# Kernel optimization log

Measured on AMD Instinct MI355X. Metric: run time of the kernel, lower is better.

## Reference

```python
import jax, jax.numpy as jnp
import numpy as np

B, T, S = 8, 8192, 128
VD, LD, E, H = 256, 768, 256, 8
HD = E // H
SCALE = HD ** -0.5
NEG = -9e15


def setup_inputs() -> dict:
    key = jax.random.key(0)
    ks = jax.random.split(key, 16)
    def xavier(k, shape):
        fan_in, fan_out = shape[1], shape[0]
        lim = np.sqrt(6.0 / (fan_in + fan_out))
        return jax.random.uniform(k, shape, jnp.float32, -lim, lim)
    return {
        "v": jax.random.normal(ks[0], (B, T, VD), jnp.float32),
        "l": jax.random.normal(ks[1], (B, S, LD), jnp.float32),
        "v_pos": jax.random.normal(ks[2], (B, T, VD), jnp.float32),
        "attention_mask_l": jnp.ones((B, S), jnp.int32),
        "attention_mask_v": jnp.ones((B, T), jnp.int32),
        "Wv": xavier(ks[3], (E, VD)),  "bv": jnp.zeros((E,), jnp.float32),
        "Wl": xavier(ks[4], (E, LD)),  "bl": jnp.zeros((E,), jnp.float32),
        "Wvv": xavier(ks[5], (E, VD)), "bvv": jnp.zeros((E,), jnp.float32),
        "Wvl": xavier(ks[6], (E, LD)), "bvl": jnp.zeros((E,), jnp.float32),
        "Wov": xavier(ks[7], (VD, E)), "bov": jnp.zeros((VD,), jnp.float32),
        "Wol": xavier(ks[8], (LD, E)), "bol": jnp.zeros((LD,), jnp.float32),
    }


def _heads(x):  # [B, N, E] -> [B, H, N, HD]
    Bn, N, _ = x.shape
    return x.reshape(Bn, N, H, HD).transpose(0, 2, 1, 3)


def reference(v, l, v_pos, attention_mask_l, attention_mask_v,
              Wv, bv, Wl, bl, Wvv, bvv, Wvl, bvl, Wov, bov, Wol, bol):
    # projections
    q = _heads(((v + v_pos) @ Wv.T + bv) * SCALE)   # [B,H,T,HD]
    k = _heads(l @ Wl.T + bl)                        # [B,H,S,HD]
    val_v = _heads(v @ Wvv.T + bvv)                  # [B,H,T,HD]
    val_l = _heads(l @ Wvl.T + bvl)                  # [B,H,S,HD]

    # shared score matrix
    attn = jnp.einsum("bhtd,bhsd->bhts", q, k)       # [B,H,T,S]

    # language -> vision direction (softmax over vision tokens T)
    attn_T = attn.transpose(0, 1, 3, 2)              # [B,H,S,T]
    attn_l = attn_T - jnp.max(attn_T, axis=-1, keepdims=True)
    mv = attention_mask_v.astype(jnp.float32)
    add_v = jnp.where(mv == 0, NEG, mv)[:, None, None, :]  # [B,1,1,T]
    attn_l = jax.nn.softmax(attn_l + add_v, axis=-1)

    # vision -> language direction (softmax over language tokens S)
    ml = attention_mask_l.astype(jnp.float32)
    add_l = jnp.where(ml == 0, NEG, ml)[:, None, None, :]  # [B,1,1,S]
    attn_v = jax.nn.softmax(attn + add_l, axis=-1)

    # dropout p=0.1 is identity in eval mode
    out_v = jnp.einsum("bhts,bhsd->bhtd", attn_v, val_l)  # [B,H,T,HD]
    out_l = jnp.einsum("bhst,bhtd->bhsd", attn_l, val_v)  # [B,H,S,HD]

    out_v = out_v.transpose(0, 2, 1, 3).reshape(B, T, E) @ Wov.T + bov
    out_l = out_l.transpose(0, 2, 1, 3).reshape(B, S, E) @ Wol.T + bol
    return out_v, out_l
```

## Files before the change

kernel.cpp:

```cpp
#include <hip/hip_runtime.h>

#define B_ 8
#define T_ 8192
#define S_ 128
#define VD_ 256
#define LD_ 768
#define E_ 256
#define H_ 8
#define HD_ 32
#define TC_ 8
#define SCALE_ 0.17677669529663687f
#define NEG_ -9.0e15f

typedef __bf16 bf16x8 __attribute__((ext_vector_type(8)));
typedef float f32x4 __attribute__((ext_vector_type(4)));
typedef unsigned int uint4v __attribute__((ext_vector_type(4)));

__device__ inline float bf2f(unsigned short u) {
    return __uint_as_float(((unsigned int)u) << 16);
}
__device__ inline unsigned short f2bf(float f) {
    unsigned int u = __float_as_uint(f);
    u = u + 0x7FFFu + ((u >> 16) & 1u);
    return (unsigned short)(u >> 16);
}
__device__ inline bf16x8 lds8(const unsigned short* p) {
    uint4v v = *reinterpret_cast<const uint4v*>(p);
    return __builtin_bit_cast(bf16x8, v);
}

template<typename T>
__device__ inline uint4v load8_as_bf16(const T* p);

template<> __device__ inline uint4v load8_as_bf16<unsigned short>(const unsigned short* p) {
    return *reinterpret_cast<const uint4v*>(p);
}
template<> __device__ inline uint4v load8_as_bf16<float>(const float* p) {
    f32x4 f0 = reinterpret_cast<const f32x4*>(p)[0];
    f32x4 f1 = reinterpret_cast<const f32x4*>(p)[1];
    uint4v r;
    #pragma unroll
    for (int jj = 0; jj < 2; ++jj) {
        r[jj]     = (unsigned int)f2bf(f0[jj*2]) | ((unsigned int)f2bf(f0[jj*2+1]) << 16);
        r[jj + 2] = (unsigned int)f2bf(f1[jj*2]) | ((unsigned int)f2bf(f1[jj*2+1]) << 16);
    }
    return r;
}
__device__ inline uint4v load8_add_as_bf16(const float* p, const float* p2) {
    f32x4 a0 = reinterpret_cast<const f32x4*>(p)[0];
    f32x4 a1 = reinterpret_cast<const f32x4*>(p)[1];
    f32x4 b0 = reinterpret_cast<const f32x4*>(p2)[0];
    f32x4 b1 = reinterpret_cast<const f32x4*>(p2)[1];
    a0 += b0; a1 += b1;
    uint4v r;
    #pragma unroll
    for (int jj = 0; jj < 2; ++jj) {
        r[jj]     = (unsigned int)f2bf(a0[jj*2]) | ((unsigned int)f2bf(a0[jj*2+1]) << 16);
        r[jj + 2] = (unsigned int)f2bf(a1[jj*2]) | ((unsigned int)f2bf(a1[jj*2+1]) << 16);
    }
    return r;
}

template<typename TA, typename TW, typename TOUT, bool HAS_A2, bool SCALED>
__global__ __launch_bounds__(256) void gemm_bt(
    const TA* __restrict__ A, const TA* __restrict__ A2,
    const TW* __restrict__ W, const float* __restrict__ bias,
    TOUT* __restrict__ C, int M, int N, int K, float scale)
{
    __shared__ __align__(16) unsigned short As[64][72];
    __shared__ __align__(16) unsigned short Ws[64][72];
    const int tid  = threadIdx.x;
    const int lane = tid & 63;
    const int w    = tid >> 6;
    const int wm   = w >> 1, wn = w & 1;
    const int m0   = blockIdx.x * 64, n0 = blockIdx.y * 64;
    const int row  = tid >> 2, c0 = tid & 3;
    const int qd   = lane >> 4, lr = lane & 15;
    const f32x4 zero = {0.f, 0.f, 0.f, 0.f};
    f32x4 acc[2][2] = {{zero, zero}, {zero, zero}};

    for (int k0 = 0; k0 < K; k0 += 64) {
        #pragma unroll
        for (int cc = 0; cc < 2; ++cc) {
            int c = c0 + cc * 4;
            const TA* pa = A + (size_t)(m0 + row) * K + k0 + c * 8;
            uint4v va;
            if constexpr (HAS_A2) {
                const TA* pa2 = A2 + (size_t)(m0 + row) * K + k0 + c * 8;
                va = load8_add_as_bf16(pa, pa2);
            } else {
                va = load8_as_bf16<TA>(pa);
            }
            *reinterpret_cast<uint4v*>(&As[row][c * 8]) = va;
            const TW* pw = W + (size_t)(n0 + row) * K + k0 + c * 8;
            *reinterpret_cast<uint4v*>(&Ws[row][c * 8]) = load8_as_bf16<TW>(pw);
        }
        __syncthreads();
        #pragma unroll
        for (int ks = 0; ks < 2; ++ks) {
            bf16x8 af[2], bfr[2];
            #pragma unroll
            for (int i = 0; i < 2; ++i)
                af[i] = lds8(&As[wm * 32 + i * 16 + lr][ks * 32 + qd * 8]);
            #pragma unroll
            for (int i = 0; i < 2; ++i)
                bfr[i] = lds8(&Ws[wn * 32 + i * 16 + lr][ks * 32 + qd * 8]);
            #pragma unroll
            for (int i = 0; i < 2; ++i)
                #pragma unroll
                for (int j = 0; j < 2; ++j)
                    acc[i][j] = __builtin_amdgcn_mfma_f32_16x16x32_bf16(
                        af[i], bfr[j], acc[i][j], 0, 0, 0);
        }
        __syncthreads();
    }
    #pragma unroll
    for (int j = 0; j < 2; ++j) {
        int col = n0 + wn * 32 + j * 16 + lr;
        float bval = bias[col];
        #pragma unroll
        for (int i = 0; i < 2; ++i) {
            int r0 = m0 + wm * 32 + i * 16 + qd * 4;
            #pragma unroll
            for (int r = 0; r < 4; ++r) {
                float v = acc[i][j][r] + bval;
                if (SCALED) v *= scale;
                if constexpr (sizeof(TOUT) == 2)
                    C[(size_t)(r0 + r) * N + col] = (TOUT)f2bf(v);
                else
                    C[(size_t)(r0 + r) * N + col] = (TOUT)v;
            }
        }
    }
}

__global__ __launch_bounds__(256) void attn_v_kernel(
    const unsigned short* __restrict__ q, const unsigned short* __restrict__ k,
    const unsigned short* __restrict__ vall, const int* __restrict__ mask_l,
    unsigned short* __restrict__ hv)
{
    __shared__ __align__(16) unsigned short Pl[64][136];
    __shared__ __align__(16) unsigned short Vt[32][136];
    const int tid  = threadIdx.x;
    const int lane = tid & 63;
    const int w    = tid >> 6;
    const int bh   = blockIdx.y, b = bh >> 3, h = bh & 7;
    const int t0   = blockIdx.x * 64;
    const int quad = lane >> 4, lr = lane & 15;
    const f32x4 zero = {0.f, 0.f, 0.f, 0.f};

    {
        int s = tid >> 1, dh = (tid & 1) * 16;
        const unsigned short* p = vall + (size_t)(b * S_ + s) * E_ + h * HD_ + dh;
        #pragma unroll
        for (int part = 0; part < 2; ++part) {
            uint4v v = reinterpret_cast<const uint4v*>(p)[part];
            #pragma unroll
            for (int jj = 0; jj < 4; ++jj) {
                unsigned int u = v[jj];
                int d = dh + part * 8 + jj * 2;
                Vt[d][s]     = (unsigned short)(u & 0xffffu);
                Vt[d + 1][s] = (unsigned short)(u >> 16);
            }
        }
    }

    bf16x8 afq = lds8(q + (size_t)(b * T_ + t0 + w * 16 + lr) * E_ + h * HD_ + quad * 8);
    f32x4 sc[8];
    #pragma unroll
    for (int n = 0; n < 8; ++n) {
        bf16x8 bk = lds8(k + (size_t)(b * S_ + n * 16 + lr) * E_ + h * HD_ + quad * 8);
        sc[n] = __builtin_amdgcn_mfma_f32_16x16x32_bf16(afq, bk, zero, 0, 0, 0);
    }
    #pragma unroll
    for (int n = 0; n < 8; ++n) {
        int s = n * 16 + lr;
        int mv = mask_l[b * S_ + s];
        float ad = (mv == 0) ? NEG_ : (float)mv;
        #pragma unroll
        for (int r = 0; r < 4; ++r) sc[n][r] += ad;
    }
    #pragma unroll
    for (int r = 0; r < 4; ++r) {
        float m = -3.0e38f;
        #pragma unroll
        for (int n = 0; n < 8; ++n) m = fmaxf(m, sc[n][r]);
        for (int off = 1; off < 16; off <<= 1) m = fmaxf(m, __shfl_xor(m, off));
        float sum = 0.f;
        #pragma unroll
        for (int n = 0; n < 8; ++n) { float e = __expf(sc[n][r] - m); sc[n][r] = e; sum += e; }
        for (int off = 1; off < 16; off <<= 1) sum += __shfl_xor(sum, off);
        float inv = 1.0f / sum;
        #pragma unroll
        for (int n = 0; n < 8; ++n) sc[n][r] *= inv;
    }
    #pragma unroll
    for (int n = 0; n < 8; ++n)
        #pragma unroll
        for (int r = 0; r < 4; ++r)
            Pl[w * 16 + quad * 4 + r][n * 16 + lr] = f2bf(sc[n][r]);
    __syncthreads();
    f32x4 av[2] = {zero, zero};
    #pragma unroll
    for (int ks = 0; ks < 4; ++ks) {
        bf16x8 ap = lds8(&Pl[w * 16 + lr][ks * 32 + quad * 8]);
        #pragma unroll
        for (int nn = 0; nn < 2; ++nn) {
            bf16x8 bv = lds8(&Vt[nn * 16 + lr][ks * 32 + quad * 8]);
            av[nn] = __builtin_amdgcn_mfma_f32_16x16x32_bf16(ap, bv, av[nn], 0, 0, 0);
        }
    }
    #pragma unroll
    for (int nn = 0; nn < 2; ++nn)
        #pragma unroll
        for (int r = 0; r < 4; ++r) {
            int t = t0 + w * 16 + quad * 4 + r;
            hv[(size_t)(b * T_ + t) * E_ + h * HD_ + nn * 16 + lr] = f2bf(av[nn][r]);
        }
}

__global__ __launch_bounds__(256) void attn_l_kernel(
    const unsigned short* __restrict__ q, const unsigned short* __restrict__ k,
    const unsigned short* __restrict__ valv, const int* __restrict__ mask_v,
    float* __restrict__ pM, float* __restrict__ pL, float* __restrict__ pA)
{
    __shared__ __align__(16) unsigned short Et[128][72];
    __shared__ __align__(16) unsigned short Vt[32][72];
    const int tid  = threadIdx.x;
    const int lane = tid & 63;
    const int w    = tid >> 6;
    const int bh   = blockIdx.y, b = bh >> 3, h = bh & 7;
    const int chunk = blockIdx.x;
    const int quad = lane >> 4, lr = lane & 15;
    const int sw0  = w * 32;
    const f32x4 zero = {0.f, 0.f, 0.f, 0.f};

    bf16x8 kf[2];
    #pragma unroll
    for (int mi = 0; mi < 2; ++mi)
        kf[mi] = lds8(k + (size_t)(b * S_ + sw0 + mi * 16 + lr) * E_ + h * HD_ + quad * 8);

    float mrun[2][4], lrun[2][4];
    #pragma unroll
    for (int mi = 0; mi < 2; ++mi)
        #pragma unroll
        for (int r = 0; r < 4; ++r) { mrun[mi][r] = -3.0e38f; lrun[mi][r] = 0.f; }
    f32x4 accl[2][2] = {{zero, zero}, {zero, zero}};

    const int titer = T_ / TC_ / 64;
    for (int it = 0; it < titer; ++it) {
        int t0 = chunk * (T_ / TC_) + it * 64;
        __syncthreads();
        {
            int t = tid >> 2, dq = tid & 3;
            const unsigned short* p = valv + (size_t)(b * T_ + t0 + t) * E_ + h * HD_ + dq * 8;
            uint4v v = *reinterpret_cast<const uint4v*>(p);
            #pragma unroll
            for (int jj = 0; jj < 4; ++jj) {
                unsigned int u = v[jj];
                Vt[dq * 8 + jj * 2][t]     = (unsigned short)(u & 0xffffu);
                Vt[dq * 8 + jj * 2 + 1][t] = (unsigned short)(u >> 16);
            }
        }
        f32x4 sc[2][4];
        #pragma unroll
        for (int n = 0; n < 4; ++n) {
            bf16x8 qf = lds8(q + (size_t)(b * T_ + t0 + n * 16 + lr) * E_ + h * HD_ + quad * 8);
            #pragma unroll
            for (int mi = 0; mi < 2; ++mi)
                sc[mi][n] = __builtin_amdgcn_mfma_f32_16x16x32_bf16(kf[mi], qf, zero, 0, 0, 0);
        }
        #pragma unroll
        for (int n = 0; n < 4; ++n) {
            int t = t0 + n * 16 + lr;
            int mv = mask_v[b * T_ + t];
            float ad = (mv == 0) ? NEG_ : (float)mv;
            #pragma unroll
            for (int mi = 0; mi < 2; ++mi)
                #pragma unroll
                for (int r = 0; r < 4; ++r) sc[mi][n][r] += ad;
        }
        #pragma unroll
        for (int mi = 0; mi < 2; ++mi)
            #pragma unroll
            for (int r = 0; r < 4; ++r) {
                float lm = -3.0e38f;
                #pragma unroll
                for (int n = 0; n < 4; ++n) lm = fmaxf(lm, sc[mi][n][r]);
                for (int off = 1; off < 16; off <<= 1) lm = fmaxf(lm, __shfl_xor(lm, off));
                float mnew = fmaxf(mrun[mi][r], lm);
                float alpha = __expf(mrun[mi][r] - mnew);
                float sum = 0.f;
                #pragma unroll
                for (int n = 0; n < 4; ++n) {
                    float e = __expf(sc[mi][n][r] - mnew); sc[mi][n][r] = e; sum += e;
                }
                for (int off = 1; off < 16; off <<= 1) sum += __shfl_xor(sum, off);
                lrun[mi][r] = lrun[mi][r] * alpha + sum;
                mrun[mi][r] = mnew;
                #pragma unroll
                for (int dn = 0; dn < 2; ++dn) accl[mi][dn][r] *= alpha;
            }
        #pragma unroll
        for (int mi = 0; mi < 2; ++mi)
            #pragma unroll
            for (int n = 0; n < 4; ++n)
                #pragma unroll
                for (int r = 0; r < 4; ++r)
                    Et[sw0 + mi * 16 + quad * 4 + r][n * 16 + lr] = f2bf(sc[mi][n][r]);
        __syncthreads();
        #pragma unroll
        for (int ks = 0; ks < 2; ++ks)
            #pragma unroll
            for (int mi = 0; mi < 2; ++mi) {
                bf16x8 ae = lds8(&Et[sw0 + mi * 16 + lr][ks * 32 + quad * 8]);
                #pragma unroll
                for (int dn = 0; dn < 2; ++dn) {
                    bf16x8 bv = lds8(&Vt[dn * 16 + lr][ks * 32 + quad * 8]);
                    accl[mi][dn] = __builtin_amdgcn_mfma_f32_16x16x32_bf16(ae, bv, accl[mi][dn], 0, 0, 0);
                }
            }
    }
    int pc = bh * TC_ + chunk;
    #pragma unroll
    for (int mi = 0; mi < 2; ++mi)
        #pragma unroll
        for (int r = 0; r < 4; ++r) {
            int s = sw0 + mi * 16 + quad * 4 + r;
            if (lr == 0) {
                pM[(size_t)pc * 128 + s] = mrun[mi][r];
                pL[(size_t)pc * 128 + s] = lrun[mi][r];
            }
            #pragma unroll
            for (int dn = 0; dn < 2; ++dn)
                pA[((size_t)pc * 128 + s) * 32 + dn * 16 + lr] = accl[mi][dn][r];
        }
}

__global__ __launch_bounds__(128) void combine_kernel(
    const float* __restrict__ pM, const float* __restrict__ pL,
    const float* __restrict__ pA, unsigned short* __restrict__ hl)
{
    int bh = blockIdx.x, b = bh >> 3, h = bh & 7;
    int s = threadIdx.x;
    float mc[TC_], wcf[TC_];
    float M = -3.0e38f;
    for (int c = 0; c < TC_; ++c) {
        mc[c] = pM[(size_t)(bh * TC_ + c) * 128 + s];
        M = fmaxf(M, mc[c]);
    }
    float L = 0.f;
    for (int c = 0; c < TC_; ++c) {
        wcf[c] = __expf(mc[c] - M);
        L += pL[(size_t)(bh * TC_ + c) * 128 + s] * wcf[c];
    }
    float inv = 1.0f / L;
    for (int d = 0; d < 32; ++d) {
        float o = 0.f;
        for (int c = 0; c < TC_; ++c)
            o += pA[((size_t)(bh * TC_ + c) * 128 + s) * 32 + d] * wcf[c];
        hl[(size_t)(b * S_ + s) * E_ + h * HD_ + d] = f2bf(o * inv);
    }
}

extern "C" void kernel_launch(void* const* d_in, const int* in_sizes, int n_in,
                              void* d_out, int out_size, void* d_ws, size_t ws_size,
                              hipStream_t stream)
{
    const float* v    = (const float*)d_in[0];
    const float* l    = (const float*)d_in[1];
    const float* vpos = (const float*)d_in[2];
    const int* mask_l = (const int*)d_in[3];
    const int* mask_v = (const int*)d_in[4];
    const float* Wv   = (const float*)d_in[5];
    const float* bv   = (const float*)d_in[6];
    const float* Wl   = (const float*)d_in[7];
    const float* bl   = (const float*)d_in[8];
    const float* Wvv  = (const float*)d_in[9];
    const float* bvv  = (const float*)d_in[10];
    const float* Wvl  = (const float*)d_in[11];
    const float* bvl  = (const float*)d_in[12];
    const float* Wov  = (const float*)d_in[13];
    const float* bov  = (const float*)d_in[14];
    const float* Wol  = (const float*)d_in[15];
    const float* bol  = (const float*)d_in[16];

    char* ws = (char*)d_ws;
    unsigned short* qbuf = (unsigned short*)(ws + 0);
    unsigned short* vbuf = (unsigned short*)(ws + 33554432);
    unsigned short* kbuf = (unsigned short*)(ws + 67108864);
    unsigned short* vall = (unsigned short*)(ws + 67633152);
    unsigned short* hl   = (unsigned short*)(ws + 68157440);
    float* pM            = (float*)(ws + 68681728);
    float* pL            = (float*)(ws + 68943872);
    float* pA            = (float*)(ws + 69206016);

    float* out_v = (float*)d_out;
    float* out_l = out_v + (size_t)B_ * T_ * VD_;

    gemm_bt<float, float, unsigned short, true,  true >
        <<<dim3(B_*T_/64, E_/64), 256, 0, stream>>>(v, vpos, Wv, bv, qbuf, B_*T_, E_, VD_, SCALE_);
    gemm_bt<float, float, unsigned short, false, false>
        <<<dim3(B_*T_/64, E_/64), 256, 0, stream>>>(v, nullptr, Wvv, bvv, vbuf, B_*T_, E_, VD_, 1.f);
    gemm_bt<float, float, unsigned short, false, false>
        <<<dim3(B_*S_/64, E_/64), 256, 0, stream>>>(l, nullptr, Wl, bl, kbuf, B_*S_, E_, LD_, 1.f);
    gemm_bt<float, float, unsigned short, false, false>
        <<<dim3(B_*S_/64, E_/64), 256, 0, stream>>>(l, nullptr, Wvl, bvl, vall, B_*S_, E_, LD_, 1.f);
    attn_l_kernel<<<dim3(TC_, B_*H_), 256, 0, stream>>>(qbuf, kbuf, vbuf, mask_v, pM, pL, pA);
    combine_kernel<<<dim3(B_*H_), 128, 0, stream>>>(pM, pL, pA, hl);
    attn_v_kernel<<<dim3(T_/64, B_*H_), 256, 0, stream>>>(qbuf, kbuf, vall, mask_l, vbuf);
    gemm_bt<unsigned short, float, float, false, false>
        <<<dim3(B_*T_/64, VD_/64), 256, 0, stream>>>(vbuf, nullptr, Wov, bov, out_v, B_*T_, VD_, E_, 1.f);
    gemm_bt<unsigned short, float, float, false, false>
        <<<dim3(B_*S_/64, LD_/64), 256, 0, stream>>>(hl, nullptr, Wol, bol, out_l, B_*S_, LD_, E_, 1.f);
}
```

Baseline: 495.2 us.

## Fuse Q and value-v projections into one kernel with pre-converted bf16 weights

Replaces the two separate vision-side projection GEMMs with a single kernel. It loads each 64-row tile of v and v+v_pos once into shared memory as bf16, and half the waves compute Q while the other half compute the value projection over the full N=256 width. The weights are converted to bf16 once per call by a small kernel and read straight from global/L2. The output projection also gets a wide-N kernel that stages A once and reuses it across all 256 columns. This removes the redundant re-reads of the fp32 v inputs across N tiles and the per-tile weight conversion, at the cost of extra small conversion launches and workspace aliasing over the pA region.

Result: faster. 455.7 us (-8.0%).

```diff
diff --git a/kernel.cpp b/kernel.cpp
--- a/kernel.cpp
+++ b/kernel.cpp
@@ -61,6 +61,13 @@
     return r;
 }
 
+__global__ __launch_bounds__(256) void cvt_w(
+    const float* __restrict__ a, unsigned short* __restrict__ o)
+{
+    int i = (blockIdx.x * 256 + threadIdx.x) * 8;
+    *reinterpret_cast<uint4v*>(o + i) = load8_as_bf16<float>(a + i);
+}
+
 template<typename TA, typename TW, typename TOUT, bool HAS_A2, bool SCALED>
 __global__ __launch_bounds__(256) void gemm_bt(
     const TA* __restrict__ A, const TA* __restrict__ A2,
@@ -130,6 +137,154 @@
                 else
                     C[(size_t)(r0 + r) * N + col] = (TOUT)v;
             }
+        }
+    }
+}
+
+__global__ __launch_bounds__(512, 4) void proj_qvv(
+    const float* __restrict__ v, const float* __restrict__ vpos,
+    const unsigned short* __restrict__ Wqb, const float* __restrict__ bq,
+    const unsigned short* __restrict__ Wvb, const float* __restrict__ bvvp,
+    unsigned short* __restrict__ qout, unsigned short* __restrict__ vvout)
+{
+    __shared__ __align__(16) unsigned short As[64][264];
+    __shared__ __align__(16) unsigned short As2[64][264];
+    const int tid  = threadIdx.x;
+    const int lane = tid & 63;
+    const int w    = tid >> 6;
+    const int grp  = w >> 2;
+    const int wn   = w & 3;
+    const int m0   = blockIdx.x * 64;
+    const int quad = lane >> 4, lr = lane & 15;
+
+    {
+        const int row = tid >> 3;
+        const int cb  = (tid & 7) * 8;
+        const float* pv = v    + (size_t)(m0 + row) * VD_ + cb;
+        const float* pp = vpos + (size_t)(m0 + row) * VD_ + cb;
+        #pragma unroll
+        for (int kq = 0; kq < 4; ++kq) {
+            f32x4 a0 = reinterpret_cast<const f32x4*>(pv + kq * 64)[0];
+            f32x4 a1 = reinterpret_cast<const f32x4*>(pv + kq * 64)[1];
+            f32x4 b0 = reinterpret_cast<const f32x4*>(pp + kq * 64)[0];
+            f32x4 b1 = reinterpret_cast<const f32x4*>(pp + kq * 64)[1];
+            f32x4 s0 = a0 + b0, s1 = a1 + b1;
+            uint4v rs, rv;
+            #pragma unroll
+            for (int jj = 0; jj < 2; ++jj) {
+                rs[jj]     = (unsigned int)f2bf(s0[jj*2]) | ((unsigned int)f2bf(s0[jj*2+1]) << 16);
+                rs[jj + 2] = (unsigned int)f2bf(s1[jj*2]) | ((unsigned int)f2bf(s1[jj*2+1]) << 16);
+                rv[jj]     = (unsigned int)f2bf(a0[jj*2]) | ((unsigned int)f2bf(a0[jj*2+1]) << 16);
+                rv[jj + 2] = (unsigned int)f2bf(a1[jj*2]) | ((unsigned int)f2bf(a1[jj*2+1]) << 16);
+            }
+            *reinterpret_cast<uint4v*>(&As [row][kq * 64 + cb]) = rs;
+            *reinterpret_cast<uint4v*>(&As2[row][kq * 64 + cb]) = rv;
+        }
+    }
+    __syncthreads();
+
+    const unsigned short (*Asel)[264] = grp ? As2 : As;
+    const unsigned short* Wsel = grp ? Wvb : Wqb;
+    f32x4 acc[4][4];
+    const f32x4 zero = {0.f, 0.f, 0.f, 0.f};
+    #pragma unroll
+    for (int i = 0; i < 4; ++i)
+        #pragma unroll
+        for (int j = 0; j < 4; ++j) acc[i][j] = zero;
+
+    #pragma unroll 2
+    for (int k0 = 0; k0 < 8; ++k0) {
+        const int kc = k0 * 32 + quad * 8;
+        bf16x8 af[4], bw[4];
+        #pragma unroll
+        for (int i = 0; i < 4; ++i)
+            af[i] = lds8(&Asel[i * 16 + lr][kc]);
+        #pragma unroll
+        for (int j = 0; j < 4; ++j)
+            bw[j] = lds8(Wsel + (size_t)(wn * 64 + j * 16 + lr) * VD_ + kc);
+        #pragma unroll
+        for (int i = 0; i < 4; ++i)
+            #pragma unroll
+            for (int j = 0; j < 4; ++j)
+                acc[i][j] = __builtin_amdgcn_mfma_f32_16x16x32_bf16(
+                    af[i], bw[j], acc[i][j], 0, 0, 0);
+    }
+
+    unsigned short* outp = grp ? vvout : qout;
+    const float* bsel    = grp ? bvvp : bq;
+    const float scl      = grp ? 1.0f : SCALE_;
+    #pragma unroll
+    for (int j = 0; j < 4; ++j) {
+        const int col = wn * 64 + j * 16 + lr;
+        const float bval = bsel[col];
+        #pragma unroll
+        for (int i = 0; i < 4; ++i) {
+            const int r0 = m0 + i * 16 + quad * 4;
+            #pragma unroll
+            for (int r = 0; r < 4; ++r)
+                outp[(size_t)(r0 + r) * E_ + col] = f2bf((acc[i][j][r] + bval) * scl);
+        }
+    }
+}
+
+__global__ __launch_bounds__(256, 4) void gemm_wide_out(
+    const unsigned short* __restrict__ A, const unsigned short* __restrict__ Wb,
+    const float* __restrict__ bias, float* __restrict__ C)
+{
+    __shared__ __align__(16) unsigned short As[64][264];
+    const int tid  = threadIdx.x;
+    const int lane = tid & 63;
+    const int wn   = tid >> 6;
+    const int m0   = blockIdx.x * 64;
+    const int quad = lane >> 4, lr = lane & 15;
+
+    {
+        const int row = tid >> 2, c = tid & 3;
+        const unsigned short* pa = A + (size_t)(m0 + row) * E_;
+        #pragma unroll
+        for (int kq = 0; kq < 8; ++kq) {
+            const int col = (kq * 4 + c) * 8;
+            *reinterpret_cast<uint4v*>(&As[row][col]) =
+                *reinterpret_cast<const uint4v*>(pa + col);
+        }
+    }
+    __syncthreads();
+
+    f32x4 acc[4][4];
+    const f32x4 zero = {0.f, 0.f, 0.f, 0.f};
+    #pragma unroll
+    for (int i = 0; i < 4; ++i)
+        #pragma unroll
+        for (int j = 0; j < 4; ++j) acc[i][j] = zero;
+
+    #pragma unroll 2
+    for (int k0 = 0; k0 < 8; ++k0) {
+        const int kc = k0 * 32 + quad * 8;
+        bf16x8 af[4], bw[4];
+        #pragma unroll
+        for (int i = 0; i < 4; ++i)
+            af[i] = lds8(&As[i * 16 + lr][kc]);
+        #pragma unroll
+        for (int j = 0; j < 4; ++j)
+            bw[j] = lds8(Wb + (size_t)(wn * 64 + j * 16 + lr) * E_ + kc);
+        #pragma unroll
+        for (int i = 0; i < 4; ++i)
+            #pragma unroll
+            for (int j = 0; j < 4; ++j)
+                acc[i][j] = __builtin_amdgcn_mfma_f32_16x16x32_bf16(
+                    af[i], bw[j], acc[i][j], 0, 0, 0);
+    }
+
+    #pragma unroll
+    for (int j = 0; j < 4; ++j) {
+        const int col = wn * 64 + j * 16 + lr;
+        const float bval = bias[col];
+        #pragma unroll
+        for (int i = 0; i < 4; ++i) {
+            const int r0 = m0 + i * 16 + quad * 4;
+            #pragma unroll
+            for (int r = 0; r < 4; ++r)
+                C[(size_t)(r0 + r) * VD_ + col] = acc[i][j][r] + bval;
         }
     }
 }
@@ -394,23 +549,30 @@
     float* pM            = (float*)(ws + 68681728);
     float* pL            = (float*)(ws + 68943872);
     float* pA            = (float*)(ws + 69206016);
+    unsigned short* Wq_bf  = (unsigned short*)(ws + 69206016);
+    unsigned short* Wvv_bf = Wq_bf + 65536;
+    unsigned short* Wov_bf = Wq_bf;
 
     float* out_v = (float*)d_out;
     float* out_l = out_v + (size_t)B_ * T_ * VD_;
 
-    gemm_bt<float, float, unsigned short, true,  true >
-        <<<dim3(B_*T_/64, E_/64), 256, 0, stream>>>(v, vpos, Wv, bv, qbuf, B_*T_, E_, VD_, SCALE_);
-    gemm_bt<float, float, unsigned short, false, false>
-        <<<dim3(B_*T_/64, E_/64), 256, 0, stream>>>(v, nullptr, Wvv, bvv, vbuf, B_*T_, E_, VD_, 1.f);
+    cvt_w<<<dim3(32), 256, 0, stream>>>(Wv,  Wq_bf);
+    cvt_w<<<dim3(32), 256, 0, stream>>>(Wvv, Wvv_bf);
+
+    proj_qvv<<<dim3(B_*T_/64), 512, 0, stream>>>(
+        v, vpos, Wq_bf, bv, Wvv_bf, bvv, qbuf, vbuf);
+
     gemm_bt<float, float, unsigned short, false, false>
         <<<dim3(B_*S_/64, E_/64), 256, 0, stream>>>(l, nullptr, Wl, bl, kbuf, B_*S_, E_, LD_, 1.f);
     gemm_bt<float, float, unsigned short, false, false>
         <<<dim3(B_*S_/64, E_/64), 256, 0, stream>>>(l, nullptr, Wvl, bvl, vall, B_*S_, E_, LD_, 1.f);
+
     attn_l_kernel<<<dim3(TC_, B_*H_), 256, 0, stream>>>(qbuf, kbuf, vbuf, mask_v, pM, pL, pA);
     combine_kernel<<<dim3(B_*H_), 128, 0, stream>>>(pM, pL, pA, hl);
+    cvt_w<<<dim3(32), 256, 0, stream>>>(Wov, Wov_bf);
     attn_v_kernel<<<dim3(T_/64, B_*H_), 256, 0, stream>>>(qbuf, kbuf, vall, mask_l, vbuf);
-    gemm_bt<unsigned short, float, float, false, false>
-        <<<dim3(B_*T_/64, VD_/64), 256, 0, stream>>>(vbuf, nullptr, Wov, bov, out_v, B_*T_, VD_, E_, 1.f);
+
+    gemm_wide_out<<<dim3(B_*T_/64), 256, 0, stream>>>(vbuf, Wov_bf, bov, out_v);
     gemm_bt<unsigned short, float, float, false, false>
         <<<dim3(B_*S_/64, LD_/64), 256, 0, stream>>>(hl, nullptr, Wol, bol, out_l, B_*S_, LD_, E_, 1.f);
 }
```

## Fuse Q and value-vision projections and use register-resident wide-N GEMMs

Applied to the files above, without the earlier changes.

Pre-converts the fp32 projection weights to bf16 in workspace, then runs a single fused kernel that computes both the Q and value projections of v. Each block loads its rows of A once into registers and sweeps all 256 output columns, streaming bf16 weights straight from global memory. The output projection uses the same full-width register-tiled approach. This removes duplicate reads of v, repeated fp32-to-bf16 weight conversion inside GEMMs, and LDS staging, at the cost of three extra small conversion launches and workspace aliasing with the pA partials buffer.

Result: no change. 490.6 us (-0.9%).

```diff
diff --git a/kernel.cpp b/kernel.cpp
--- a/kernel.cpp
+++ b/kernel.cpp
@@ -24,6 +24,11 @@
     u = u + 0x7FFFu + ((u >> 16) & 1u);
     return (unsigned short)(u >> 16);
 }
+__device__ inline unsigned int pkbf(float lo, float hi) {
+    unsigned short a = __builtin_bit_cast(unsigned short, (__bf16)lo);
+    unsigned short b = __builtin_bit_cast(unsigned short, (__bf16)hi);
+    return (unsigned int)a | ((unsigned int)b << 16);
+}
 __device__ inline bf16x8 lds8(const unsigned short* p) {
     uint4v v = *reinterpret_cast<const uint4v*>(p);
     return __builtin_bit_cast(bf16x8, v);
@@ -59,6 +64,13 @@
         r[jj + 2] = (unsigned int)f2bf(a1[jj*2]) | ((unsigned int)f2bf(a1[jj*2+1]) << 16);
     }
     return r;
+}
+
+__global__ __launch_bounds__(256) void cvt_w(
+    const float* __restrict__ a, unsigned short* __restrict__ o)
+{
+    int i = (blockIdx.x * 256 + threadIdx.x) * 8;
+    *reinterpret_cast<uint4v*>(o + i) = load8_as_bf16<float>(a + i);
 }
 
 template<typename TA, typename TW, typename TOUT, bool HAS_A2, bool SCALED>
@@ -130,6 +142,104 @@
                 else
                     C[(size_t)(r0 + r) * N + col] = (TOUT)v;
             }
+        }
+    }
+}
+
+__global__ __launch_bounds__(256, 4) void proj_qvv(
+    const float* __restrict__ v, const float* __restrict__ vpos,
+    const unsigned short* __restrict__ Wqb, const float* __restrict__ bq,
+    const unsigned short* __restrict__ Wvb, const float* __restrict__ bvvp,
+    unsigned short* __restrict__ qout, unsigned short* __restrict__ vvout)
+{
+    const int tid  = threadIdx.x;
+    const int lane = tid & 63;
+    const int w    = tid >> 6;
+    const int grp  = w >> 1;
+    const int r0   = blockIdx.x * 64 + (w & 1) * 32;
+    const int quad = lane >> 4, lr = lane & 15;
+
+    bf16x8 af[2][8];
+    #pragma unroll
+    for (int i = 0; i < 2; ++i) {
+        const float* pv = v    + (size_t)(r0 + i * 16 + lr) * VD_ + quad * 8;
+        const float* pp = vpos + (size_t)(r0 + i * 16 + lr) * VD_ + quad * 8;
+        #pragma unroll
+        for (int kq = 0; kq < 8; ++kq) {
+            f32x4 a0 = reinterpret_cast<const f32x4*>(pv + kq * 32)[0];
+            f32x4 a1 = reinterpret_cast<const f32x4*>(pv + kq * 32)[1];
+            if (grp == 0) {
+                f32x4 b0 = reinterpret_cast<const f32x4*>(pp + kq * 32)[0];
+                f32x4 b1 = reinterpret_cast<const f32x4*>(pp + kq * 32)[1];
+                a0 += b0; a1 += b1;
+            }
+            uint4v u;
+            u[0] = pkbf(a0[0], a0[1]); u[1] = pkbf(a0[2], a0[3]);
+            u[2] = pkbf(a1[0], a1[1]); u[3] = pkbf(a1[2], a1[3]);
+            af[i][kq] = __builtin_bit_cast(bf16x8, u);
+        }
+    }
+
+    const unsigned short* Wsel = grp ? Wvb : Wqb;
+    const float* bsel          = grp ? bvvp : bq;
+    unsigned short* outp       = grp ? vvout : qout;
+    const float scl            = grp ? 1.0f : SCALE_;
+    const f32x4 zero = {0.f, 0.f, 0.f, 0.f};
+
+    #pragma unroll 2
+    for (int j = 0; j < 16; ++j) {
+        const unsigned short* wp = Wsel + (size_t)(j * 16 + lr) * VD_ + quad * 8;
+        f32x4 acc0 = zero, acc1 = zero;
+        #pragma unroll
+        for (int kq = 0; kq < 8; ++kq) {
+            bf16x8 bw = lds8(wp + kq * 32);
+            acc0 = __builtin_amdgcn_mfma_f32_16x16x32_bf16(af[0][kq], bw, acc0, 0, 0, 0);
+            acc1 = __builtin_amdgcn_mfma_f32_16x16x32_bf16(af[1][kq], bw, acc1, 0, 0, 0);
+        }
+        const float bval = bsel[j * 16 + lr];
+        #pragma unroll
+        for (int r = 0; r < 4; ++r) {
+            outp[(size_t)(r0 + quad * 4 + r) * E_ + j * 16 + lr]      = f2bf((acc0[r] + bval) * scl);
+            outp[(size_t)(r0 + 16 + quad * 4 + r) * E_ + j * 16 + lr] = f2bf((acc1[r] + bval) * scl);
+        }
+    }
+}
+
+__global__ __launch_bounds__(256, 4) void gemm_wide_out(
+    const unsigned short* __restrict__ A, const unsigned short* __restrict__ Wb,
+    const float* __restrict__ bias, float* __restrict__ C)
+{
+    const int tid  = threadIdx.x;
+    const int lane = tid & 63;
+    const int w    = tid >> 6;
+    const int quad = lane >> 4, lr = lane & 15;
+    const int r0   = blockIdx.x * 128 + w * 32;
+
+    bf16x8 af[2][8];
+    #pragma unroll
+    for (int i = 0; i < 2; ++i) {
+        const unsigned short* pa = A + (size_t)(r0 + i * 16 + lr) * E_ + quad * 8;
+        #pragma unroll
+        for (int kq = 0; kq < 8; ++kq)
+            af[i][kq] = lds8(pa + kq * 32);
+    }
+    const f32x4 zero = {0.f, 0.f, 0.f, 0.f};
+
+    #pragma unroll 2
+    for (int j = 0; j < 16; ++j) {
+        const unsigned short* wp = Wb + (size_t)(j * 16 + lr) * E_ + quad * 8;
+        f32x4 acc0 = zero, acc1 = zero;
+        #pragma unroll
+        for (int kq = 0; kq < 8; ++kq) {
+            bf16x8 bw = lds8(wp + kq * 32);
+            acc0 = __builtin_amdgcn_mfma_f32_16x16x32_bf16(af[0][kq], bw, acc0, 0, 0, 0);
+            acc1 = __builtin_amdgcn_mfma_f32_16x16x32_bf16(af[1][kq], bw, acc1, 0, 0, 0);
+        }
+        const float bval = bias[j * 16 + lr];
+        #pragma unroll
+        for (int r = 0; r < 4; ++r) {
+            C[(size_t)(r0 + quad * 4 + r) * VD_ + j * 16 + lr]      = acc0[r] + bval;
+            C[(size_t)(r0 + 16 + quad * 4 + r) * VD_ + j * 16 + lr] = acc1[r] + bval;
         }
     }
 }
@@ -394,23 +504,30 @@
     float* pM            = (float*)(ws + 68681728);
     float* pL            = (float*)(ws + 68943872);
     float* pA            = (float*)(ws + 69206016);
+    unsigned short* Wq_bf  = (unsigned short*)(ws + 69206016);
+    unsigned short* Wvv_bf = Wq_bf + 65536;
+    unsigned short* Wov_bf = Wq_bf;
 
     float* out_v = (float*)d_out;
     float* out_l = out_v + (size_t)B_ * T_ * VD_;
 
-    gemm_bt<float, float, unsigned short, true,  true >
-        <<<dim3(B_*T_/64, E_/64), 256, 0, stream>>>(v, vpos, Wv, bv, qbuf, B_*T_, E_, VD_, SCALE_);
-    gemm_bt<float, float, unsigned short, false, false>
-        <<<dim3(B_*T_/64, E_/64), 256, 0, stream>>>(v, nullptr, Wvv, bvv, vbuf, B_*T_, E_, VD_, 1.f);
+    cvt_w<<<dim3(32), 256, 0, stream>>>(Wv,  Wq_bf);
+    cvt_w<<<dim3(32), 256, 0, stream>>>(Wvv, Wvv_bf);
+
+    proj_qvv<<<dim3(B_*T_/64), 256, 0, stream>>>(
+        v, vpos, Wq_bf, bv, Wvv_bf, bvv, qbuf, vbuf);
+
     gemm_bt<float, float, unsigned short, false, false>
         <<<dim3(B_*S_/64, E_/64), 256, 0, stream>>>(l, nullptr, Wl, bl, kbuf, B_*S_, E_, LD_, 1.f);
     gemm_bt<float, float, unsigned short, false, false>
         <<<dim3(B_*S_/64, E_/64), 256, 0, stream>>>(l, nullptr, Wvl, bvl, vall, B_*S_, E_, LD_, 1.f);
+
     attn_l_kernel<<<dim3(TC_, B_*H_), 256, 0, stream>>>(qbuf, kbuf, vbuf, mask_v, pM, pL, pA);
     combine_kernel<<<dim3(B_*H_), 128, 0, stream>>>(pM, pL, pA, hl);
+    cvt_w<<<dim3(32), 256, 0, stream>>>(Wov, Wov_bf);
     attn_v_kernel<<<dim3(T_/64, B_*H_), 256, 0, stream>>>(qbuf, kbuf, vall, mask_l, vbuf);
-    gemm_bt<unsigned short, float, float, false, false>
-        <<<dim3(B_*T_/64, VD_/64), 256, 0, stream>>>(vbuf, nullptr, Wov, bov, out_v, B_*T_, VD_, E_, 1.f);
+
+    gemm_wide_out<<<dim3(B_*T_/128), 256, 0, stream>>>(vbuf, Wov_bf, bov, out_v);
     gemm_bt<unsigned short, float, float, false, false>
         <<<dim3(B_*S_/64, LD_/64), 256, 0, stream>>>(hl, nullptr, Wol, bol, out_l, B_*S_, LD_, E_, 1.f);
 }
```

## Add weight-stationary GEMM holding full 256x256 bf16 weight in LDS for large projections

Applied to the files above, without the earlier changes.

Adds a gemm_ws kernel that loads the entire 256x256 weight matrix into LDS as swizzled bf16. Each 512-thread block handles 256 rows and keeps its A fragments in registers across all output columns. It replaces the tiled gemm_bt for the q, val_v and out_v projections, so A is read once and the weight is not re-streamed through K-loop tiles. The cost is 128KB of LDS per block, which limits occupancy to one block per CU. Each block also reconverts the fp32 weight to bf16, and the output stores are narrow per-element writes.

Measured after the change: 445.2 us. -10.1%, faster.

```diff
diff --git a/kernel.cpp b/kernel.cpp
--- a/kernel.cpp
+++ b/kernel.cpp
@@ -23,6 +23,11 @@
     unsigned int u = __float_as_uint(f);
     u = u + 0x7FFFu + ((u >> 16) & 1u);
     return (unsigned short)(u >> 16);
+}
+__device__ inline unsigned int pkbf(float lo, float hi) {
+    unsigned short a = __builtin_bit_cast(unsigned short, (__bf16)lo);
+    unsigned short b = __builtin_bit_cast(unsigned short, (__bf16)hi);
+    return (unsigned int)a | ((unsigned int)b << 16);
 }
 __device__ inline bf16x8 lds8(const unsigned short* p) {
     uint4v v = *reinterpret_cast<const uint4v*>(p);
@@ -129,6 +134,89 @@
                     C[(size_t)(r0 + r) * N + col] = (TOUT)f2bf(v);
                 else
                     C[(size_t)(r0 + r) * N + col] = (TOUT)v;
+            }
+        }
+    }
+}
+
+template<typename TA, typename TOUT, bool HAS_A2, bool SCALED>
+__global__ __launch_bounds__(512) void gemm_ws(
+    const TA* __restrict__ A, const float* __restrict__ A2,
+    const float* __restrict__ Wf, const float* __restrict__ bias,
+    TOUT* __restrict__ C, float scale)
+{
+    __shared__ __align__(16) unsigned short Ws[256 * 256];
+    const int tid  = threadIdx.x;
+    const int lane = tid & 63;
+    const int w    = tid >> 6;
+    const int quad = lane >> 4, lr = lane & 15;
+
+    {
+        const int row = tid >> 1;
+        const int gb  = (tid & 1) * 16;
+        #pragma unroll 8
+        for (int i = 0; i < 16; ++i) {
+            const int g  = gb + i;
+            const int gs = g ^ (row & 7);
+            uint4v val = load8_as_bf16<float>(Wf + (size_t)row * 256 + g * 8);
+            *reinterpret_cast<uint4v*>(&Ws[row * 256 + gs * 8]) = val;
+        }
+    }
+
+    const int r0 = blockIdx.x * 256 + w * 32;
+    bf16x8 af[2][8];
+    #pragma unroll
+    for (int i = 0; i < 2; ++i) {
+        const int row = r0 + i * 16 + lr;
+        #pragma unroll
+        for (int kq = 0; kq < 8; ++kq) {
+            if constexpr (sizeof(TA) == 2) {
+                af[i][kq] = lds8(reinterpret_cast<const unsigned short*>(A)
+                                 + (size_t)row * 256 + quad * 8 + kq * 32);
+            } else {
+                const float* pa = reinterpret_cast<const float*>(A)
+                                  + (size_t)row * 256 + quad * 8 + kq * 32;
+                f32x4 a0 = reinterpret_cast<const f32x4*>(pa)[0];
+                f32x4 a1 = reinterpret_cast<const f32x4*>(pa)[1];
+                if constexpr (HAS_A2) {
+                    const float* pp = A2 + (size_t)row * 256 + quad * 8 + kq * 32;
+                    a0 += reinterpret_cast<const f32x4*>(pp)[0];
+                    a1 += reinterpret_cast<const f32x4*>(pp)[1];
+                }
+                uint4v u;
+                u[0] = pkbf(a0[0], a0[1]); u[1] = pkbf(a0[2], a0[3]);
+                u[2] = pkbf(a1[0], a1[1]); u[3] = pkbf(a1[2], a1[3]);
+                af[i][kq] = __builtin_bit_cast(bf16x8, u);
+            }
+        }
+    }
+    __syncthreads();
+
+    const f32x4 zero = {0.f, 0.f, 0.f, 0.f};
+    const int swz = lr & 7;
+    for (int j = 0; j < 16; ++j) {
+        const unsigned short* wbase = &Ws[(j * 16 + lr) * 256];
+        f32x4 acc0 = zero, acc1 = zero;
+        #pragma unroll
+        for (int kq = 0; kq < 8; ++kq) {
+            const int gs = (kq * 4 + quad) ^ swz;
+            bf16x8 bw = lds8(wbase + gs * 8);
+            acc0 = __builtin_amdgcn_mfma_f32_16x16x32_bf16(af[0][kq], bw, acc0, 0, 0, 0);
+            acc1 = __builtin_amdgcn_mfma_f32_16x16x32_bf16(af[1][kq], bw, acc1, 0, 0, 0);
+        }
+        const int col = j * 16 + lr;
+        const float bval = bias[col];
+        #pragma unroll
+        for (int r = 0; r < 4; ++r) {
+            float v0 = acc0[r] + bval;
+            float v1 = acc1[r] + bval;
+            if constexpr (SCALED) { v0 *= scale; v1 *= scale; }
+            if constexpr (sizeof(TOUT) == 2) {
+                C[(size_t)(r0 + quad * 4 + r) * 256 + col]      = (TOUT)f2bf(v0);
+                C[(size_t)(r0 + 16 + quad * 4 + r) * 256 + col] = (TOUT)f2bf(v1);
+            } else {
+                C[(size_t)(r0 + quad * 4 + r) * 256 + col]      = (TOUT)v0;
+                C[(size_t)(r0 + 16 + quad * 4 + r) * 256 + col] = (TOUT)v1;
             }
         }
     }
@@ -398,19 +486,22 @@
     float* out_v = (float*)d_out;
     float* out_l = out_v + (size_t)B_ * T_ * VD_;
 
-    gemm_bt<float, float, unsigned short, true,  true >
-        <<<dim3(B_*T_/64, E_/64), 256, 0, stream>>>(v, vpos, Wv, bv, qbuf, B_*T_, E_, VD_, SCALE_);
-    gemm_bt<float, float, unsigned short, false, false>
-        <<<dim3(B_*T_/64, E_/64), 256, 0, stream>>>(v, nullptr, Wvv, bvv, vbuf, B_*T_, E_, VD_, 1.f);
+    gemm_ws<float, unsigned short, true, true>
+        <<<dim3(B_*T_/256), 512, 0, stream>>>(v, vpos, Wv, bv, qbuf, SCALE_);
+    gemm_ws<float, unsigned short, false, false>
+        <<<dim3(B_*T_/256), 512, 0, stream>>>(v, nullptr, Wvv, bvv, vbuf, 1.f);
+
     gemm_bt<float, float, unsigned short, false, false>
         <<<dim3(B_*S_/64, E_/64), 256, 0, stream>>>(l, nullptr, Wl, bl, kbuf, B_*S_, E_, LD_, 1.f);
     gemm_bt<float, float, unsigned short, false, false>
         <<<dim3(B_*S_/64, E_/64), 256, 0, stream>>>(l, nullptr, Wvl, bvl, vall, B_*S_, E_, LD_, 1.f);
+
     attn_l_kernel<<<dim3(TC_, B_*H_), 256, 0, stream>>>(qbuf, kbuf, vbuf, mask_v, pM, pL, pA);
     combine_kernel<<<dim3(B_*H_), 128, 0, stream>>>(pM, pL, pA, hl);
     attn_v_kernel<<<dim3(T_/64, B_*H_), 256, 0, stream>>>(qbuf, kbuf, vall, mask_l, vbuf);
-    gemm_bt<unsigned short, float, float, false, false>
-        <<<dim3(B_*T_/64, VD_/64), 256, 0, stream>>>(vbuf, nullptr, Wov, bov, out_v, B_*T_, VD_, E_, 1.f);
+
+    gemm_ws<unsigned short, float, false, false>
+        <<<dim3(B_*T_/256), 512, 0, stream>>>(vbuf, nullptr, Wov, bov, out_v, 1.f);
     gemm_bt<unsigned short, float, float, false, false>
         <<<dim3(B_*S_/64, LD_/64), 256, 0, stream>>>(hl, nullptr, Wol, bol, out_l, B_*S_, LD_, E_, 1.f);
 }
```
